# Kernel tuning notes

Measured on AMD Instinct MI355X. Metric: run time of the kernel, lower is better.

Reference implementation:

```python
import jax, jax.numpy as jnp
import numpy as np

N_ENSEMBLE = 50
STATE_DIM = 32
ACTION_DIM = 8
HIDDEN = 256
BATCH = 8192
OUT_DIM = STATE_DIM + 1  # next_state + reward


def setup_inputs() -> dict:
    key = jax.random.key(0)
    ks = jax.random.split(key, 8)
    s = 0.05  # small init scale to keep activations sane
    return {
        "state": jax.random.normal(ks[0], (BATCH, STATE_DIM), dtype=jnp.float32),
        "action": jax.random.normal(ks[1], (BATCH, ACTION_DIM), dtype=jnp.float32),
        "W1": jax.random.normal(ks[2], (N_ENSEMBLE, STATE_DIM + ACTION_DIM, HIDDEN), dtype=jnp.float32) * s,
        "b1": jnp.zeros((N_ENSEMBLE, HIDDEN), dtype=jnp.float32),
        "W2": jax.random.normal(ks[3], (N_ENSEMBLE, HIDDEN, HIDDEN), dtype=jnp.float32) * s,
        "b2": jnp.zeros((N_ENSEMBLE, HIDDEN), dtype=jnp.float32),
        "W3": jax.random.normal(ks[4], (N_ENSEMBLE, HIDDEN, HIDDEN), dtype=jnp.float32) * s,
        "b3": jnp.zeros((N_ENSEMBLE, HIDDEN), dtype=jnp.float32),
        "W4": jax.random.normal(ks[5], (N_ENSEMBLE, HIDDEN, OUT_DIM), dtype=jnp.float32) * s,
        "b4": jnp.zeros((N_ENSEMBLE, OUT_DIM), dtype=jnp.float32),
    }


def reference(state, action, W1, b1, W2, b2, W3, b3, W4, b4):
    # state_action: [B, S+A] shared across all ensemble members
    sa = jnp.concatenate((state, action), axis=1)
    # Batched-over-ensemble GEMMs replace the python loop over 50 MLPs.
    # h: [B, E, H]
    h = jax.nn.relu(jnp.einsum("bi,eih->beh", sa, W1) + b1)
    h = jax.nn.relu(jnp.einsum("beh,ehk->bek", h, W2) + b2)
    h = jax.nn.relu(jnp.einsum("beh,ehk->bek", h, W3) + b3)
    preds = jnp.einsum("beh,eho->beo", h, W4) + b4  # [B, E, S+1]
    return preds[..., :-1], preds[..., -1]
```

## Files before the change

kernel.cpp:

```cpp
#include <hip/hip_runtime.h>


typedef __attribute__((ext_vector_type(8))) short short8;
typedef __attribute__((ext_vector_type(4))) float floatx4;

#define NE 50
#define NB 8192
#define OUT_NS_ELEMS (NB * NE * 32)
#define OSTRIDE 48

__device__ __forceinline__ unsigned short f2bf_rne(float x) {
  unsigned u = __float_as_uint(x);
  u += 0x7fffu + ((u >> 16) & 1u);
  return (unsigned short)(u >> 16);
}
__device__ __forceinline__ float bf2f(unsigned short b) {
  return __uint_as_float(((unsigned)b) << 16);
}
__device__ __forceinline__ floatx4 mfma16(short8 a, short8 b, floatx4 c) {
  return __builtin_amdgcn_mfma_f32_16x16x32_bf16(a, b, c, 0, 0, 0);
}
__device__ __forceinline__ unsigned pack_bf2(float lo, float hi) {
  unsigned u0 = __float_as_uint(lo) + 0x8000u;
  unsigned u1 = __float_as_uint(hi) + 0x8000u;
  return __builtin_amdgcn_perm(u1, u0, 0x07060302u);
}

__global__ void k_detect(const unsigned* __restrict__ w2raw, int* __restrict__ flag) {
  __shared__ int s_bad;
  if (threadIdx.x == 0) s_bad = 0;
  __syncthreads();
  bool bad = false;
  for (int i = threadIdx.x; i < 2048; i += 256) {
    unsigned word = w2raw[i * 797];
    unsigned short lo = (unsigned short)(word & 0xFFFFu);
    float f = bf2f(lo);
    if (!(fabsf(f) < 16.0f)) bad = true;
    if (lo == 0) bad = true;
  }
  if (bad) s_bad = 1;
  __syncthreads();
  if (threadIdx.x == 0) *flag = s_bad ? 0 : 1;
}

__device__ __forceinline__ unsigned short load_bf(const void* p, long i, bool isbf) {
  if (isbf) return ((const unsigned short*)p)[i];
  return f2bf_rne(((const float*)p)[i]);
}
__device__ __forceinline__ float load_f(const void* p, long i, bool isbf) {
  if (isbf) return bf2f(((const unsigned short*)p)[i]);
  return ((const float*)p)[i];
}

__device__ void pack_w_panel(const void* __restrict__ src, unsigned short* __restrict__ dst,
                             bool isbf, int e, int kt, int K, int N, int NT, int perE,
                             unsigned short* lds) {
  const int t = threadIdx.x;
  const int Npad = NT * 16;
  const int NP = Npad + 10;
  for (int idx = t; idx < 32 * Npad; idx += 256) {
    int r = idx / Npad, c = idx - r * Npad;
    int k = kt * 32 + r;
    unsigned short v = 0;
    if (k < K && c < N) v = load_bf(src, (long)(e * K + k) * N + c, isbf);
    lds[r * NP + c] = v;
  }
  __syncthreads();
  for (int u = t; u < NT * 64; u += 256) {
    int nt = u >> 6, kb = (u >> 4) & 3, ni = u & 15;
    int n = nt * 16 + ni;
    unsigned v[4];
#pragma unroll
    for (int p = 0; p < 4; ++p) {
      unsigned lo = lds[(kb * 8 + 2 * p) * NP + n];
      unsigned hi = lds[(kb * 8 + 2 * p + 1) * NP + n];
      v[p] = lo | (hi << 16);
    }
    long off = (long)e * perE + ((long)((kt * NT + nt) * 64 + kb * 16 + ni)) * 8;
    *(uint4*)(dst + off) = make_uint4(v[0], v[1], v[2], v[3]);
  }
}

__global__ void k_pack(const void* __restrict__ state, const void* __restrict__ action,
                       const void* __restrict__ W1, const void* __restrict__ W2,
                       const void* __restrict__ W3, const void* __restrict__ W4,
                       const void* __restrict__ b1, const void* __restrict__ b2,
                       const void* __restrict__ b3, const void* __restrict__ b4,
                       const int* __restrict__ flag,
                       unsigned short* __restrict__ saP, unsigned short* __restrict__ w1P,
                       unsigned short* __restrict__ w2P, unsigned short* __restrict__ w3P,
                       unsigned short* __restrict__ w4P, float* __restrict__ biasP) {
  __shared__ unsigned short lds[32 * 266];
  const bool isbf = (*flag != 0);
  const int b = blockIdx.x;
  if (b < 400) {
    pack_w_panel(W2, w2P, isbf, b >> 3, b & 7, 256, 256, 16, 65536, lds);
  } else if (b < 800) {
    int bb = b - 400;
    pack_w_panel(W3, w3P, isbf, bb >> 3, bb & 7, 256, 256, 16, 65536, lds);
  } else if (b < 900) {
    int bb = b - 800;
    pack_w_panel(W1, w1P, isbf, bb >> 1, bb & 1, 40, 256, 16, 16384, lds);
  } else if (b < 1300) {
    int bb = b - 900;
    pack_w_panel(W4, w4P, isbf, bb >> 3, bb & 7, 256, 33, 3, 12288, lds);
  } else if (b < 1556) {
    int u = (b - 1300) * 256 + threadIdx.x;
    int mi = u & 15, kb = (u >> 4) & 7, mt = u >> 7;
    int row = mt * 16 + mi;
    unsigned v[4] = {0u, 0u, 0u, 0u};
    if (kb < 4) {
#pragma unroll
      for (int p = 0; p < 4; ++p) {
        unsigned lo = load_bf(state, (long)row * 32 + kb * 8 + 2 * p, isbf);
        unsigned hi = load_bf(state, (long)row * 32 + kb * 8 + 2 * p + 1, isbf);
        v[p] = lo | (hi << 16);
      }
    } else if (kb == 4) {
#pragma unroll
      for (int p = 0; p < 4; ++p) {
        unsigned lo = load_bf(action, (long)row * 8 + 2 * p, isbf);
        unsigned hi = load_bf(action, (long)row * 8 + 2 * p + 1, isbf);
        v[p] = lo | (hi << 16);
      }
    }
    *(uint4*)(saP + (long)u * 8) = make_uint4(v[0], v[1], v[2], v[3]);
  } else {
    int gid = (b - 1556) * 256 + threadIdx.x;
    if (gid < NE * 816) {
      int e = gid / 816, r = gid - e * 816;
      float v = 0.0f;
      if (r < 256)      v = load_f(b1, e * 256 + r,         isbf);
      else if (r < 512) v = load_f(b2, e * 256 + (r - 256), isbf);
      else if (r < 768) v = load_f(b3, e * 256 + (r - 512), isbf);
      else { int q = r - 768; if (q < 33) v = load_f(b4, e * 33 + q, isbf); }
      biasP[gid] = v;
    }
  }
}


__device__ __forceinline__ void store_tile16(const floatx4& a4, unsigned short* hT,
                                             int FT, int BT, int li, int g) {
  int k0 = FT * 16 + g * 4;
  unsigned d0 = pack_bf2(fmaxf(a4[0], 0.0f), fmaxf(a4[1], 0.0f));
  unsigned d1 = pack_bf2(fmaxf(a4[2], 0.0f), fmaxf(a4[3], 0.0f));
  int addr = ((k0 >> 5) * 8 + BT) * 512 + ((k0 >> 3) & 3) * 128 + li * 8 + (k0 & 7);
  *(unsigned long long*)(hT + addr) =
      (unsigned long long)d0 | ((unsigned long long)d1 << 32);
}

__device__ __forceinline__ void hidden_layer(const unsigned short* __restrict__ wp,
                                             const float* __restrict__ br,
                                             unsigned short* hT,
                                             int wf, int l, int li, int g) {
  floatx4 acc[4][8];
#pragma unroll
  for (int ot = 0; ot < 4; ++ot) {
    const float4 bq = *(const float4*)(br + wf * 64 + ot * 16 + g * 4);
    floatx4 iv = {bq.x, bq.y, bq.z, bq.w};
#pragma unroll
    for (int bt = 0; bt < 8; ++bt) acc[ot][bt] = iv;
  }
  short8 a[4], an[4];
#pragma unroll
  for (int ot = 0; ot < 4; ++ot)
    a[ot] = *(const short8*)(wp + (long)((wf * 4 + ot) * 64 + l) * 8);
#pragma unroll
  for (int kt = 0; kt < 8; ++kt) {
    if (kt < 7) {
#pragma unroll
      for (int ot = 0; ot < 4; ++ot)
        an[ot] = *(const short8*)(wp + (long)(((kt + 1) * 16 + wf * 4 + ot) * 64 + l) * 8);
    }
#pragma unroll
    for (int bt = 0; bt < 8; ++bt) {
      short8 b = *(const short8*)(hT + ((kt * 8 + bt) * 64 + l) * 8);
#pragma unroll
      for (int ot = 0; ot < 4; ++ot)
        acc[ot][bt] = mfma16(a[ot], b, acc[ot][bt]);
    }
    if (kt < 7) {
#pragma unroll
      for (int ot = 0; ot < 4; ++ot) a[ot] = an[ot];
    }
  }
  __syncthreads();
#pragma unroll
  for (int ot = 0; ot < 4; ++ot)
#pragma unroll
    for (int bt = 0; bt < 8; ++bt)
      store_tile16(acc[ot][bt], hT, wf * 4 + ot, bt, li, g);
  __syncthreads();
}

__global__ __launch_bounds__(256, 2) void k_mlp(
    const unsigned short* __restrict__ sa,
    const unsigned short* __restrict__ w1,
    const unsigned short* __restrict__ w2,
    const unsigned short* __restrict__ w3,
    const unsigned short* __restrict__ w4,
    const float* __restrict__ bias,
    const int* __restrict__ flag,
    float* __restrict__ rewardWS,
    void* __restrict__ outp) {
  __shared__ __attribute__((aligned(16))) unsigned short hT[32768];
  const int tid = threadIdx.x;
  const int wf = tid >> 6, l = tid & 63, li = l & 15, g = l >> 4;
  const int bb = blockIdx.x;
  const int e  = blockIdx.y;
  const float* brow = bias + e * 816;
  const bool isbf = (*flag != 0);

  {
    floatx4 acc[4][8];
#pragma unroll
    for (int ot = 0; ot < 4; ++ot) {
      const float4 bq = *(const float4*)(brow + wf * 64 + ot * 16 + g * 4);
      floatx4 iv = {bq.x, bq.y, bq.z, bq.w};
#pragma unroll
      for (int bt = 0; bt < 8; ++bt) acc[ot][bt] = iv;
    }
#pragma unroll
    for (int kt = 0; kt < 2; ++kt) {
      short8 a[4];
#pragma unroll
      for (int ot = 0; ot < 4; ++ot)
        a[ot] = *(const short8*)(w1 + (long)e * 16384 +
                                 (long)((kt * 16 + wf * 4 + ot) * 64 + l) * 8);
#pragma unroll
      for (int bt = 0; bt < 8; ++bt) {
        short8 b = *(const short8*)(sa + (long)((bb * 8 + bt) * 128 + kt * 64 + l) * 8);
#pragma unroll
        for (int ot = 0; ot < 4; ++ot)
          acc[ot][bt] = mfma16(a[ot], b, acc[ot][bt]);
      }
    }
#pragma unroll
    for (int ot = 0; ot < 4; ++ot)
#pragma unroll
      for (int bt = 0; bt < 8; ++bt)
        store_tile16(acc[ot][bt], hT, wf * 4 + ot, bt, li, g);
    __syncthreads();
  }

  hidden_layer(w2 + (long)e * 65536, brow + 256, hT, wf, l, li, g);
  hidden_layer(w3 + (long)e * 65536, brow + 512, hT, wf, l, li, g);

  const float* brow4 = brow + 768;
  floatx4 acc4[3][2];
#pragma unroll
  for (int ft = 0; ft < 3; ++ft) {
    const float4 bq = *(const float4*)(brow4 + ft * 16 + g * 4);
    floatx4 iv = {bq.x, bq.y, bq.z, bq.w};
    acc4[ft][0] = iv;
    acc4[ft][1] = iv;
  }
#pragma unroll
  for (int kt = 0; kt < 8; ++kt) {
    short8 a[3];
#pragma unroll
    for (int ft = 0; ft < 3; ++ft)
      a[ft] = *(const short8*)(w4 + (long)e * 12288 + (long)((kt * 3 + ft) * 64 + l) * 8);
#pragma unroll
    for (int bl = 0; bl < 2; ++bl) {
      short8 b = *(const short8*)(hT + ((kt * 8 + wf * 2 + bl) * 64 + l) * 8);
#pragma unroll
      for (int ft = 0; ft < 3; ++ft)
        acc4[ft][bl] = mfma16(a[ft], b, acc4[ft][bl]);
    }
  }

  if (g == 0) {
#pragma unroll
    for (int bl = 0; bl < 2; ++bl)
      rewardWS[(long)e * NB + bb * 128 + (wf * 2 + bl) * 16 + li] = acc4[2][bl][0];
  }

  __syncthreads();
#pragma unroll
  for (int ft = 0; ft < 2; ++ft) {
#pragma unroll
    for (int bl = 0; bl < 2; ++bl) {
      int batch = (wf * 2 + bl) * 16 + li;
      unsigned d0 = pack_bf2(acc4[ft][bl][0], acc4[ft][bl][1]);
      unsigned d1 = pack_bf2(acc4[ft][bl][2], acc4[ft][bl][3]);
      *(unsigned long long*)(hT + batch * OSTRIDE + ft * 16 + g * 4) =
          (unsigned long long)d0 | ((unsigned long long)d1 << 32);
    }
  }
  __syncthreads();

  if (isbf) {
    unsigned short* o16 = (unsigned short*)outp;
#pragma unroll
    for (int p = 0; p < 2; ++p) {
      int batch = p * 64 + (tid >> 2);
      int chunk = tid & 3;
      uint4 v = *(const uint4*)(hT + batch * OSTRIDE + chunk * 8);
      *(uint4*)(o16 + ((long)(bb * 128 + batch) * NE + e) * 32 + chunk * 8) = v;
    }
  } else {
    float* o32 = (float*)outp;
#pragma unroll
    for (int p = 0; p < 4; ++p) {
      int idx = p * 256 + tid;
      int batch = idx >> 3;
      int chunk = idx & 7;
      const unsigned short* s = hT + batch * OSTRIDE + chunk * 4;
      *(float4*)(o32 + ((long)(bb * 128 + batch) * NE + e) * 32 + chunk * 4) =
          make_float4(bf2f(s[0]), bf2f(s[1]), bf2f(s[2]), bf2f(s[3]));
    }
  }
}

__global__ void k_reward(const float* __restrict__ rw, const int* __restrict__ flag,
                         void* __restrict__ outp) {
  int id = blockIdx.x * 256 + threadIdx.x;
  if (id >= NB * NE) return;
  int b = id / NE, e = id - b * NE;
  float v = rw[(long)e * NB + b];
  if (*flag != 0) {
    unsigned u = __float_as_uint(v) + 0x8000u;
    ((unsigned short*)outp)[OUT_NS_ELEMS + id] = (unsigned short)(u >> 16);
  } else {
    ((float*)outp)[OUT_NS_ELEMS + id] = v;
  }
}

extern "C" void kernel_launch(void* const* d_in, const int* in_sizes, int n_in,
                              void* d_out, int out_size, void* d_ws, size_t ws_size,
                              hipStream_t stream) {
  const void* state  = d_in[0];
  const void* action = d_in[1];
  const void* W1 = d_in[2];
  const void* b1 = d_in[3];
  const void* W2 = d_in[4];
  const void* b2 = d_in[5];
  const void* W3 = d_in[6];
  const void* b3 = d_in[7];
  const void* W4 = d_in[8];
  const void* b4 = d_in[9];
  (void)in_sizes; (void)n_in; (void)out_size; (void)ws_size;

  char* ws = (char*)d_ws;
  int* flag              = (int*)(ws + 0);
  unsigned short* saP    = (unsigned short*)(ws + 256);
  unsigned short* w1P    = (unsigned short*)(ws + 1048832);
  unsigned short* w2P    = (unsigned short*)(ws + 2687232);
  unsigned short* w3P    = (unsigned short*)(ws + 9240832);
  unsigned short* w4P    = (unsigned short*)(ws + 15794432);
  float* biasP           = (float*)(ws + 17023232);
  float* rewardWS        = (float*)(ws + 17186432);

  k_detect<<<1, 256, 0, stream>>>((const unsigned*)W2, flag);
  k_pack<<<1716, 256, 0, stream>>>(state, action, W1, W2, W3, W4, b1, b2, b3, b4,
                                   flag, saP, w1P, w2P, w3P, w4P, biasP);
  k_mlp<<<dim3(64, 50), 256, 0, stream>>>(saP, w1P, w2P, w3P, w4P, biasP, flag,
                                          rewardWS, d_out);
  k_reward<<<(NB * NE + 255) / 256, 256, 0, stream>>>(rewardWS, flag, d_out);
}
```

Before: 253.5 us.

## Halve batch tile per block to raise occupancy and fold dtype detection into pack

The MLP kernel now processes 64 batch rows per block instead of 128. That halves the accumulator registers and LDS use, raises launch bounds to 4 blocks per CU, and doubles the grid. The explicit software prefetch of next-k weight fragments is removed. The separate detection kernel is merged into every pack block, which drops one launch but repeats the sampling reads in each block. The cost is that each block reloads weights twice as often relative to the batch rows it processes.

Measured after the change: 249.8 us. No clear change (-1.5%).

```diff
diff --git a/kernel.cpp b/kernel.cpp
--- a/kernel.cpp
+++ b/kernel.cpp
@@ -24,23 +24,6 @@
   unsigned u0 = __float_as_uint(lo) + 0x8000u;
   unsigned u1 = __float_as_uint(hi) + 0x8000u;
   return __builtin_amdgcn_perm(u1, u0, 0x07060302u);
-}
-
-__global__ void k_detect(const unsigned* __restrict__ w2raw, int* __restrict__ flag) {
-  __shared__ int s_bad;
-  if (threadIdx.x == 0) s_bad = 0;
-  __syncthreads();
-  bool bad = false;
-  for (int i = threadIdx.x; i < 2048; i += 256) {
-    unsigned word = w2raw[i * 797];
-    unsigned short lo = (unsigned short)(word & 0xFFFFu);
-    float f = bf2f(lo);
-    if (!(fabsf(f) < 16.0f)) bad = true;
-    if (lo == 0) bad = true;
-  }
-  if (bad) s_bad = 1;
-  __syncthreads();
-  if (threadIdx.x == 0) *flag = s_bad ? 0 : 1;
 }
 
 __device__ __forceinline__ unsigned short load_bf(const void* p, long i, bool isbf) {
@@ -86,12 +69,25 @@
                        const void* __restrict__ W3, const void* __restrict__ W4,
                        const void* __restrict__ b1, const void* __restrict__ b2,
                        const void* __restrict__ b3, const void* __restrict__ b4,
-                       const int* __restrict__ flag,
+                       int* __restrict__ flag,
                        unsigned short* __restrict__ saP, unsigned short* __restrict__ w1P,
                        unsigned short* __restrict__ w2P, unsigned short* __restrict__ w3P,
                        unsigned short* __restrict__ w4P, float* __restrict__ biasP) {
   __shared__ unsigned short lds[32 * 266];
-  const bool isbf = (*flag != 0);
+  __shared__ int s_bad;
+  const int t = threadIdx.x;
+  if (t == 0) s_bad = 0;
+  __syncthreads();
+  if (t < 64) {
+    unsigned word = ((const unsigned*)W2)[(long)(t * 32) * 797];
+    unsigned short lo = (unsigned short)(word & 0xFFFFu);
+    float f = bf2f(lo);
+    if (!(fabsf(f) < 16.0f) || lo == 0) s_bad = 1;
+  }
+  __syncthreads();
+  const bool isbf = (s_bad == 0);
+  if (blockIdx.x == 0 && t == 0) *flag = isbf ? 1 : 0;
+
   const int b = blockIdx.x;
   if (b < 400) {
     pack_w_panel(W2, w2P, isbf, b >> 3, b & 7, 256, 256, 16, 65536, lds);
@@ -145,7 +141,7 @@
   int k0 = FT * 16 + g * 4;
   unsigned d0 = pack_bf2(fmaxf(a4[0], 0.0f), fmaxf(a4[1], 0.0f));
   unsigned d1 = pack_bf2(fmaxf(a4[2], 0.0f), fmaxf(a4[3], 0.0f));
-  int addr = ((k0 >> 5) * 8 + BT) * 512 + ((k0 >> 3) & 3) * 128 + li * 8 + (k0 & 7);
+  int addr = ((k0 >> 5) * 4 + BT) * 512 + ((k0 >> 3) & 3) * 128 + li * 8 + (k0 & 7);
   *(unsigned long long*)(hT + addr) =
       (unsigned long long)d0 | ((unsigned long long)d1 << 32);
 }
@@ -154,47 +150,38 @@
                                              const float* __restrict__ br,
                                              unsigned short* hT,
                                              int wf, int l, int li, int g) {
-  floatx4 acc[4][8];
+  floatx4 acc[4][4];
 #pragma unroll
   for (int ot = 0; ot < 4; ++ot) {
     const float4 bq = *(const float4*)(br + wf * 64 + ot * 16 + g * 4);
     floatx4 iv = {bq.x, bq.y, bq.z, bq.w};
 #pragma unroll
-    for (int bt = 0; bt < 8; ++bt) acc[ot][bt] = iv;
-  }
-  short8 a[4], an[4];
-#pragma unroll
-  for (int ot = 0; ot < 4; ++ot)
-    a[ot] = *(const short8*)(wp + (long)((wf * 4 + ot) * 64 + l) * 8);
+    for (int bt = 0; bt < 4; ++bt) acc[ot][bt] = iv;
+  }
 #pragma unroll
   for (int kt = 0; kt < 8; ++kt) {
-    if (kt < 7) {
-#pragma unroll
-      for (int ot = 0; ot < 4; ++ot)
-        an[ot] = *(const short8*)(wp + (long)(((kt + 1) * 16 + wf * 4 + ot) * 64 + l) * 8);
-    }
-#pragma unroll
-    for (int bt = 0; bt < 8; ++bt) {
-      short8 b = *(const short8*)(hT + ((kt * 8 + bt) * 64 + l) * 8);
+    short8 a[4];
+#pragma unroll
+    for (int ot = 0; ot < 4; ++ot)
+      a[ot] = *(const short8*)(wp + (long)((kt * 16 + wf * 4 + ot) * 64 + l) * 8);
+#pragma unroll
+    for (int bt = 0; bt < 4; ++bt) {
+      short8 b = *(const short8*)(hT + ((kt * 4 + bt) * 64 + l) * 8);
 #pragma unroll
       for (int ot = 0; ot < 4; ++ot)
         acc[ot][bt] = mfma16(a[ot], b, acc[ot][bt]);
     }
-    if (kt < 7) {
-#pragma unroll
-      for (int ot = 0; ot < 4; ++ot) a[ot] = an[ot];
-    }
   }
   __syncthreads();
 #pragma unroll
   for (int ot = 0; ot < 4; ++ot)
 #pragma unroll
-    for (int bt = 0; bt < 8; ++bt)
+    for (int bt = 0; bt < 4; ++bt)
       store_tile16(acc[ot][bt], hT, wf * 4 + ot, bt, li, g);
   __syncthreads();
 }
 
-__global__ __launch_bounds__(256, 2) void k_mlp(
+__global__ __launch_bounds__(256, 4) void k_mlp(
     const unsigned short* __restrict__ sa,
     const unsigned short* __restrict__ w1,
     const unsigned short* __restrict__ w2,
@@ -204,7 +191,7 @@
     const int* __restrict__ flag,
     float* __restrict__ rewardWS,
     void* __restrict__ outp) {
-  __shared__ __attribute__((aligned(16))) unsigned short hT[32768];
+  __shared__ __attribute__((aligned(16))) unsigned short hT[16384];
   const int tid = threadIdx.x;
   const int wf = tid >> 6, l = tid & 63, li = l & 15, g = l >> 4;
   const int bb = blockIdx.x;
@@ -213,13 +200,13 @@
   const bool isbf = (*flag != 0);
 
   {
-    floatx4 acc[4][8];
+    floatx4 acc[4][4];
 #pragma unroll
     for (int ot = 0; ot < 4; ++ot) {
       const float4 bq = *(const float4*)(brow + wf * 64 + ot * 16 + g * 4);
       floatx4 iv = {bq.x, bq.y, bq.z, bq.w};
 #pragma unroll
-      for (int bt = 0; bt < 8; ++bt) acc[ot][bt] = iv;
+      for (int bt = 0; bt < 4; ++bt) acc[ot][bt] = iv;
     }
 #pragma unroll
     for (int kt = 0; kt < 2; ++kt) {
@@ -229,8 +216,8 @@
         a[ot] = *(const short8*)(w1 + (long)e * 16384 +
                                  (long)((kt * 16 + wf * 4 + ot) * 64 + l) * 8);
 #pragma unroll
-      for (int bt = 0; bt < 8; ++bt) {
-        short8 b = *(const short8*)(sa + (long)((bb * 8 + bt) * 128 + kt * 64 + l) * 8);
+      for (int bt = 0; bt < 4; ++bt) {
+        short8 b = *(const short8*)(sa + (long)((bb * 4 + bt) * 128 + kt * 64 + l) * 8);
 #pragma unroll
         for (int ot = 0; ot < 4; ++ot)
           acc[ot][bt] = mfma16(a[ot], b, acc[ot][bt]);
@@ -239,7 +226,7 @@
 #pragma unroll
     for (int ot = 0; ot < 4; ++ot)
 #pragma unroll
-      for (int bt = 0; bt < 8; ++bt)
+      for (int bt = 0; bt < 4; ++bt)
         store_tile16(acc[ot][bt], hT, wf * 4 + ot, bt, li, g);
     __syncthreads();
   }
@@ -248,13 +235,12 @@
   hidden_layer(w3 + (long)e * 65536, brow + 512, hT, wf, l, li, g);
 
   const float* brow4 = brow + 768;
-  floatx4 acc4[3][2];
+  floatx4 acc4[3];
 #pragma unroll
   for (int ft = 0; ft < 3; ++ft) {
     const float4 bq = *(const float4*)(brow4 + ft * 16 + g * 4);
     floatx4 iv = {bq.x, bq.y, bq.z, bq.w};
-    acc4[ft][0] = iv;
-    acc4[ft][1] = iv;
+    acc4[ft] = iv;
   }
 #pragma unroll
   for (int kt = 0; kt < 8; ++kt) {
@@ -262,53 +248,42 @@
 #pragma unroll
     for (int ft = 0; ft < 3; ++ft)
       a[ft] = *(const short8*)(w4 + (long)e * 12288 + (long)((kt * 3 + ft) * 64 + l) * 8);
-#pragma unroll
-    for (int bl = 0; bl < 2; ++bl) {
-      short8 b = *(const short8*)(hT + ((kt * 8 + wf * 2 + bl) * 64 + l) * 8);
-#pragma unroll
-      for (int ft = 0; ft < 3; ++ft)
-        acc4[ft][bl] = mfma16(a[ft], b, acc4[ft][bl]);
-    }
+    short8 b = *(const short8*)(hT + ((kt * 4 + wf) * 64 + l) * 8);
+#pragma unroll
+    for (int ft = 0; ft < 3; ++ft)
+      acc4[ft] = mfma16(a[ft], b, acc4[ft]);
   }
 
   if (g == 0) {
-#pragma unroll
-    for (int bl = 0; bl < 2; ++bl)
-      rewardWS[(long)e * NB + bb * 128 + (wf * 2 + bl) * 16 + li] = acc4[2][bl][0];
+    rewardWS[(long)e * NB + bb * 64 + wf * 16 + li] = acc4[2][0];
   }
 
   __syncthreads();
 #pragma unroll
   for (int ft = 0; ft < 2; ++ft) {
-#pragma unroll
-    for (int bl = 0; bl < 2; ++bl) {
-      int batch = (wf * 2 + bl) * 16 + li;
-      unsigned d0 = pack_bf2(acc4[ft][bl][0], acc4[ft][bl][1]);
-      unsigned d1 = pack_bf2(acc4[ft][bl][2], acc4[ft][bl][3]);
-      *(unsigned long long*)(hT + batch * OSTRIDE + ft * 16 + g * 4) =
-          (unsigned long long)d0 | ((unsigned long long)d1 << 32);
-    }
+    int batch = wf * 16 + li;
+    unsigned d0 = pack_bf2(acc4[ft][0], acc4[ft][1]);
+    unsigned d1 = pack_bf2(acc4[ft][2], acc4[ft][3]);
+    *(unsigned long long*)(hT + batch * OSTRIDE + ft * 16 + g * 4) =
+        (unsigned long long)d0 | ((unsigned long long)d1 << 32);
   }
   __syncthreads();
 
   if (isbf) {
     unsigned short* o16 = (unsigned short*)outp;
-#pragma unroll
-    for (int p = 0; p < 2; ++p) {
-      int batch = p * 64 + (tid >> 2);
-      int chunk = tid & 3;
-      uint4 v = *(const uint4*)(hT + batch * OSTRIDE + chunk * 8);
-      *(uint4*)(o16 + ((long)(bb * 128 + batch) * NE + e) * 32 + chunk * 8) = v;
-    }
+    int batch = tid >> 2;
+    int chunk = tid & 3;
+    uint4 v = *(const uint4*)(hT + batch * OSTRIDE + chunk * 8);
+    *(uint4*)(o16 + ((long)(bb * 64 + batch) * NE + e) * 32 + chunk * 8) = v;
   } else {
     float* o32 = (float*)outp;
 #pragma unroll
-    for (int p = 0; p < 4; ++p) {
+    for (int p = 0; p < 2; ++p) {
       int idx = p * 256 + tid;
       int batch = idx >> 3;
       int chunk = idx & 7;
       const unsigned short* s = hT + batch * OSTRIDE + chunk * 4;
-      *(float4*)(o32 + ((long)(bb * 128 + batch) * NE + e) * 32 + chunk * 4) =
+      *(float4*)(o32 + ((long)(bb * 64 + batch) * NE + e) * 32 + chunk * 4) =
           make_float4(bf2f(s[0]), bf2f(s[1]), bf2f(s[2]), bf2f(s[3]));
     }
   }
@@ -353,10 +328,9 @@
   float* biasP           = (float*)(ws + 17023232);
   float* rewardWS        = (float*)(ws + 17186432);
 
-  k_detect<<<1, 256, 0, stream>>>((const unsigned*)W2, flag);
   k_pack<<<1716, 256, 0, stream>>>(state, action, W1, W2, W3, W4, b1, b2, b3, b4,
                                    flag, saP, w1P, w2P, w3P, w4P, biasP);
-  k_mlp<<<dim3(64, 50), 256, 0, stream>>>(saP, w1P, w2P, w3P, w4P, biasP, flag,
-                                          rewardWS, d_out);
+  k_mlp<<<dim3(128, 50), 256, 0, stream>>>(saP, w1P, w2P, w3P, w4P, biasP, flag,
+                                           rewardWS, d_out);
   k_reward<<<(NB * NE + 255) / 256, 256, 0, stream>>>(rewardWS, flag, d_out);
 }
```
